# Performance work log

Hardware: AMD Instinct MI355X
Metric: run time of the kernel (lower is better)

Reference implementation:

```python
import jax, jax.numpy as jnp
import numpy as np

HID = 64
NUM_LAYERS = 4
IN_DIM = 1
OUT_DIM = 1
LN_EPS = 1e-5


def setup_inputs() -> dict:
    key = jax.random.key(0)
    ks = jax.random.split(key, 2 * NUM_LAYERS + 5)
    B, S = 1024, 512
    inp = {"x": jax.random.normal(ks[0], (B, S, IN_DIM), dtype=jnp.float32)}
    # per-layer gate weights, stored as [in+H, 4H] (x @ W + b, equivalent to torch Linear)
    for l in range(NUM_LAYERS):
        in_dim = IN_DIM if l == 0 else HID
        fan_in = in_dim + HID
        bound = 1.0 / np.sqrt(fan_in)
        inp[f"W{l}"] = jax.random.uniform(ks[1 + 2 * l], (fan_in, 4 * HID), jnp.float32, -bound, bound)
        inp[f"b{l}"] = jax.random.uniform(ks[2 + 2 * l], (4 * HID,), jnp.float32, -bound, bound)
    inp["ln_g"] = jnp.ones((HID,), jnp.float32)
    inp["ln_b"] = jnp.zeros((HID,), jnp.float32)
    bo = 1.0 / np.sqrt(HID)
    inp["Wout"] = jax.random.uniform(ks[-2], (HID, OUT_DIM), jnp.float32, -bo, bo)
    inp["bout"] = jax.random.uniform(ks[-1], (OUT_DIM,), jnp.float32, -bo, bo)
    return inp


def _lstm_forward(x, Ws, bs):
    B = x.shape[0]
    h0 = tuple(jnp.zeros((B, HID), x.dtype) for _ in range(NUM_LAYERS))
    c0 = tuple(jnp.zeros((B, HID), x.dtype) for _ in range(NUM_LAYERS))

    def step(carry, xt):
        h, c = carry
        inp = xt
        new_h, new_c = [], []
        for l in range(NUM_LAYERS):
            z = jnp.concatenate([inp, h[l]], axis=-1) @ Ws[l] + bs[l]  # [B, 4H]
            i, f, g, o = jnp.split(z, 4, axis=-1)
            i = jax.nn.sigmoid(i)
            f = jax.nn.sigmoid(f)
            g = jnp.tanh(g)
            o = jax.nn.sigmoid(o)
            c_new = f * c[l] + i * g
            h_new = o * jnp.tanh(c_new)
            new_h.append(h_new)
            new_c.append(c_new)
            inp = h_new
        return (tuple(new_h), tuple(new_c)), new_h[-1]

    xs = jnp.swapaxes(x, 0, 1)  # [S, B, in]
    _, outs = jax.lax.scan(step, (h0, c0), xs)
    return jnp.swapaxes(outs, 0, 1)  # [B, S, H]


def reference(x, W0, b0, W1, b1, W2, b2, W3, b3, ln_g, ln_b, Wout, bout):
    Ws = (W0, W1, W2, W3)
    bs = (b0, b1, b2, b3)
    out = _lstm_forward(x, Ws, bs)  # [B, S, H]
    mu = jnp.mean(out, axis=-1, keepdims=True)
    var = jnp.mean(jnp.square(out - mu), axis=-1, keepdims=True)
    normed = (out - mu) * jax.lax.rsqrt(var + LN_EPS) * ln_g + ln_b
    return normed @ Wout + bout  # [B, S, 1]
```

## Files before the change

kernel.cpp:

```cpp
#include <hip/hip_runtime.h>

#define SEQ   512
#define NTHR  1024
#define NBLK  256

typedef _Float16 f16x8 __attribute__((ext_vector_type(8)));
typedef float    f32x4 __attribute__((ext_vector_type(4)));

#define MFMA(a, b, c) __builtin_amdgcn_mfma_f32_16x16x32_f16((a), (b), (c), 0, 0, 0)

__device__ __forceinline__ float sig_(float x) {
    return __builtin_amdgcn_rcpf(1.0f + __builtin_amdgcn_exp2f(x * -1.4426950408889634f));
}
__device__ __forceinline__ float tanh_(float x) {
    return fmaf(2.0f, __builtin_amdgcn_rcpf(1.0f + __builtin_amdgcn_exp2f(x * -2.8853900817779268f)), -1.0f);
}

__global__ __launch_bounds__(NTHR, 4) void lstm4_pipe16b(
    const float* __restrict__ x,
    const float* __restrict__ W0, const float* __restrict__ B0,
    const float* __restrict__ W1, const float* __restrict__ B1,
    const float* __restrict__ W2, const float* __restrict__ B2,
    const float* __restrict__ W3, const float* __restrict__ B3,
    const float* __restrict__ ln_g, const float* __restrict__ ln_b,
    const float* __restrict__ Wout, const float* __restrict__ bout,
    float* __restrict__ out)
{
    __shared__ __align__(16) _Float16 hbuf[2][4][4][64];
    __shared__ float xall[4][SEQ];
    __shared__ float part[16][4][4][3];
    __shared__ float sconst[2];

    const int tid  = threadIdx.x;
    const int lane = tid & 63;
    const int w    = tid >> 6;
    const int ell  = w >> 2;
    const int om   = w & 3;
    const int lam  = lane >> 4;
    const int bc   = lane & 15;
    const int br   = bc & 3;
    const int k    = bc >> 2;
    const int bb   = blockIdx.x;

    for (int i = tid; i < 4 * SEQ; i += NTHR)
        xall[i >> 9][i & 511] = x[bb * 4 * SEQ + i];
    for (int i = tid; i < 2 * 4 * 4 * 64; i += NTHR)
        ((_Float16*)hbuf)[i] = (_Float16)0.0f;

    if (tid < 64) {
        float a = ln_g[tid] * Wout[tid];
        float b = ln_b[tid] * Wout[tid];
#pragma unroll
        for (int off = 32; off > 0; off >>= 1) {
            a += __shfl_xor(a, off, 64);
            b += __shfl_xor(b, off, 64);
        }
        if (tid == 0) { sconst[0] = a; sconst[1] = b; }
    }

    const float* Wp = (ell == 0) ? W0 : (ell == 1) ? W1 : (ell == 2) ? W2 : W3;
    const float* Bp = (ell == 0) ? B0 : (ell == 1) ? B1 : (ell == 2) ? B2 : B3;

    f16x8 wf[4][4];
    f32x4 biasv[4];
#pragma unroll
    for (int i = 0; i < 4; ++i) {
        const int T  = om * 4 + i;
        const int cA = (bc & 3) * 64 + T * 4 + (bc >> 2);
        if (ell == 0) {
#pragma unroll
            for (int kt = 0; kt < 2; ++kt)
#pragma unroll
                for (int e = 0; e < 8; ++e)
                    wf[i][kt][e] = (_Float16)W0[(1 + kt * 32 + lam * 8 + e) * 256 + cA];
#pragma unroll
            for (int e = 0; e < 8; ++e) { wf[i][2][e] = (_Float16)0.0f; wf[i][3][e] = (_Float16)0.0f; }
            if (lam == 0) wf[i][2][0] = (_Float16)W0[cA];
        } else {
#pragma unroll
            for (int kt = 0; kt < 4; ++kt)
#pragma unroll
                for (int e = 0; e < 8; ++e)
                    wf[i][kt][e] = (_Float16)Wp[(kt * 32 + lam * 8 + e) * 256 + cA];
        }
#pragma unroll
        for (int r = 0; r < 4; ++r)
            biasv[i][r] = Bp[r * 64 + T * 4 + lam];
    }

    const int   mK  = (om * 4 + k) * 4 + lam;
    const float gwK = ln_g[mK] * Wout[mK];
    const int   wrK = br * 128 + (((mK >> 3) ^ br) * 16) + (mK & 7) * 2;

    const int a0 = br * 128 + ((lam)     ^ br) * 16;
    const int a1 = br * 128 + ((4 + lam) ^ br) * 16;

    const bool k1b = (bc & 4) != 0;
    const bool k2b = (bc & 8) != 0;

    float cstK = 0.0f;
    char* const hb = (char*)hbuf;

    __syncthreads();
    const float Sgw = sconst[0];
    const float Sbw = sconst[1] + bout[0];

    for (int tau = 0; tau < SEQ + 3; ++tau) {
        const char* bR = hb + (((tau + 1) & 1) ? 2048 : 0);
        char*       bW = hb + (((tau    ) & 1) ? 2048 : 0);
        const int  t      = tau - ell;
        const bool active = (t >= 0) && (t < SEQ);

        if (active) {
            f16x8 b0, b1, b2, b3;
            if (ell == 0) {
                b0 = *(const f16x8*)(bR + a0);
                b1 = *(const f16x8*)(bR + a1);
                f16x8 xf;
#pragma unroll
                for (int e = 0; e < 8; ++e) xf[e] = (_Float16)0.0f;
                if (lam == 0) xf[0] = (_Float16)xall[br][t];
                b2 = xf; b3 = xf;
            } else {
                const char* bIn   = bR + (ell - 1) * 512;
                const char* bSelf = bR + ell * 512;
                b0 = *(const f16x8*)(bIn + a0);
                b1 = *(const f16x8*)(bIn + a1);
                b2 = *(const f16x8*)(bSelf + a0);
                b3 = *(const f16x8*)(bSelf + a1);
            }

            f32x4 A0 = MFMA(wf[0][0], b0, biasv[0]);
            f32x4 A1 = MFMA(wf[1][0], b0, biasv[1]);
            f32x4 A2 = MFMA(wf[2][0], b0, biasv[2]);
            f32x4 A3 = MFMA(wf[3][0], b0, biasv[3]);
            A0 = MFMA(wf[0][1], b1, A0);  A1 = MFMA(wf[1][1], b1, A1);
            A2 = MFMA(wf[2][1], b1, A2);  A3 = MFMA(wf[3][1], b1, A3);
            A0 = MFMA(wf[0][2], b2, A0);  A1 = MFMA(wf[1][2], b2, A1);
            A2 = MFMA(wf[2][2], b2, A2);  A3 = MFMA(wf[3][2], b2, A3);
            A0 = MFMA(wf[0][3], b3, A0);  A1 = MFMA(wf[1][3], b3, A1);
            A2 = MFMA(wf[2][3], b3, A2);  A3 = MFMA(wf[3][3], b3, A3);

            const f32x4 s01 = k1b ? A1 : A0;
            const f32x4 s23 = k1b ? A3 : A2;
            const f32x4 aK  = k2b ? s23 : s01;

            const float gi = sig_(aK[0]);
            const float gf = sig_(aK[1]);
            const float gg = tanh_(aK[2]);
            const float go = sig_(aK[3]);
            cstK = fmaf(gf, cstK, gi * gg);
            const float hn = go * tanh_(cstK);
            *(_Float16*)(bW + ell * 512 + wrK) = (_Float16)hn;

            if (ell == 3) {
                float v1 = hn, v2 = hn * hn, v3 = hn * gwK;
                v1 += __shfl_xor(v1, 4, 64);  v2 += __shfl_xor(v2, 4, 64);  v3 += __shfl_xor(v3, 4, 64);
                v1 += __shfl_xor(v1, 8, 64);  v2 += __shfl_xor(v2, 8, 64);  v3 += __shfl_xor(v3, 8, 64);
                v1 += __shfl_xor(v1, 16, 64); v2 += __shfl_xor(v2, 16, 64); v3 += __shfl_xor(v3, 16, 64);
                v1 += __shfl_xor(v1, 32, 64); v2 += __shfl_xor(v2, 32, 64); v3 += __shfl_xor(v3, 32, 64);
                if (bc < 4) {
                    float* pp = &part[t & 15][om][bc][0];
                    pp[0] = v1; pp[1] = v2; pp[2] = v3;
                }
            }
        }
        __syncthreads();

        const int t3 = tau - 3;
        if (t3 >= 7 && (t3 & 7) == 7) {
            const int row = tid >> 4, sub = tid & 15;
            if (row < 32) {
                const int sl = row >> 2, b = row & 3;
                const int slot = (t3 - 7 + sl) & 15;
                float u1 = part[slot][sub & 3][b][0];
                float u2 = part[slot][sub & 3][b][1];
                float u3 = part[slot][sub & 3][b][2];
                u1 += __shfl_xor(u1, 1, 64); u2 += __shfl_xor(u2, 1, 64); u3 += __shfl_xor(u3, 1, 64);
                u1 += __shfl_xor(u1, 2, 64); u2 += __shfl_xor(u2, 2, 64); u3 += __shfl_xor(u3, 2, 64);
                if (sub == 0) {
                    const float mu = u1 * (1.0f / 64.0f);
                    float var = fmaf(u2, 1.0f / 64.0f, -mu * mu);
                    var = fmaxf(var, 0.0f);
                    const float rs = rsqrtf(var + 1e-5f);
                    out[(bb * 4 + b) * SEQ + (t3 - 7) + sl] = fmaf(rs, fmaf(-mu, Sgw, u3), Sbw);
                }
            }
        }
    }
}

extern "C" void kernel_launch(void* const* d_in, const int* in_sizes, int n_in,
                              void* d_out, int out_size, void* d_ws, size_t ws_size,
                              hipStream_t stream)
{
    const float* x    = (const float*)d_in[0];
    const float* W0   = (const float*)d_in[1];
    const float* B0   = (const float*)d_in[2];
    const float* W1   = (const float*)d_in[3];
    const float* B1   = (const float*)d_in[4];
    const float* W2   = (const float*)d_in[5];
    const float* B2   = (const float*)d_in[6];
    const float* W3   = (const float*)d_in[7];
    const float* B3   = (const float*)d_in[8];
    const float* ln_g = (const float*)d_in[9];
    const float* ln_b = (const float*)d_in[10];
    const float* Wout = (const float*)d_in[11];
    const float* bout = (const float*)d_in[12];
    float* out = (float*)d_out;

    lstm4_pipe16b<<<NBLK, NTHR, 0, stream>>>(x, W0, B0, W1, B1, W2, B2, W3, B3,
                                             ln_g, ln_b, Wout, bout, out);
}
```

Measured before the change: 560.6 us.

## Give each wave a whole LSTM layer with a deeper skewed pipeline

The block shrinks from 16 waves to 4, so each wave owns one full layer and computes all 16 gate tiles sequentially. The layer stagger grows to two steps, and the hidden state moves to a 4-slot LDS ring, so a block barrier is needed only every other step. The layer-norm and output projection are now done inside the last-layer wave with shuffles, which removes the shared partial-sum buffer and the separate reduction phase. In exchange each wave holds 4x the weight registers, which risks spills or AGPR use, and there is less wave-level parallelism to hide MFMA and transcendental latency.

```diff
diff --git a/kernel.cpp b/kernel.cpp
--- a/kernel.cpp
+++ b/kernel.cpp
@@ -1,7 +1,7 @@
 #include <hip/hip_runtime.h>
 
 #define SEQ   512
-#define NTHR  1024
+#define NTHR  256
 #define NBLK  256
 
 typedef _Float16 f16x8 __attribute__((ext_vector_type(8)));
@@ -16,7 +16,7 @@
     return fmaf(2.0f, __builtin_amdgcn_rcpf(1.0f + __builtin_amdgcn_exp2f(x * -2.8853900817779268f)), -1.0f);
 }
 
-__global__ __launch_bounds__(NTHR, 4) void lstm4_pipe16b(
+__global__ __launch_bounds__(NTHR, 1) void lstm4_deep(
     const float* __restrict__ x,
     const float* __restrict__ W0, const float* __restrict__ B0,
     const float* __restrict__ W1, const float* __restrict__ B1,
@@ -26,25 +26,22 @@
     const float* __restrict__ Wout, const float* __restrict__ bout,
     float* __restrict__ out)
 {
-    __shared__ __align__(16) _Float16 hbuf[2][4][4][64];
+    __shared__ __align__(16) _Float16 hbuf[4][4][4][64];
     __shared__ float xall[4][SEQ];
-    __shared__ float part[16][4][4][3];
     __shared__ float sconst[2];
 
     const int tid  = threadIdx.x;
     const int lane = tid & 63;
-    const int w    = tid >> 6;
-    const int ell  = w >> 2;
-    const int om   = w & 3;
+    const int ell  = tid >> 6;
     const int lam  = lane >> 4;
     const int bc   = lane & 15;
     const int br   = bc & 3;
-    const int k    = bc >> 2;
+    const int kq   = bc >> 2;
     const int bb   = blockIdx.x;
 
     for (int i = tid; i < 4 * SEQ; i += NTHR)
         xall[i >> 9][i & 511] = x[bb * 4 * SEQ + i];
-    for (int i = tid; i < 2 * 4 * 4 * 64; i += NTHR)
+    for (int i = tid; i < 4 * 4 * 4 * 64; i += NTHR)
         ((_Float16*)hbuf)[i] = (_Float16)0.0f;
 
     if (tid < 64) {
@@ -61,132 +58,125 @@
     const float* Wp = (ell == 0) ? W0 : (ell == 1) ? W1 : (ell == 2) ? W2 : W3;
     const float* Bp = (ell == 0) ? B0 : (ell == 1) ? B1 : (ell == 2) ? B2 : B3;
 
-    f16x8 wf[4][4];
-    f32x4 biasv[4];
-#pragma unroll
-    for (int i = 0; i < 4; ++i) {
-        const int T  = om * 4 + i;
+    f16x8 wf[16][4];
+    f32x4 biasv[16];
+#pragma unroll
+    for (int T = 0; T < 16; ++T) {
         const int cA = (bc & 3) * 64 + T * 4 + (bc >> 2);
         if (ell == 0) {
 #pragma unroll
             for (int kt = 0; kt < 2; ++kt)
 #pragma unroll
                 for (int e = 0; e < 8; ++e)
-                    wf[i][kt][e] = (_Float16)W0[(1 + kt * 32 + lam * 8 + e) * 256 + cA];
-#pragma unroll
-            for (int e = 0; e < 8; ++e) { wf[i][2][e] = (_Float16)0.0f; wf[i][3][e] = (_Float16)0.0f; }
-            if (lam == 0) wf[i][2][0] = (_Float16)W0[cA];
+                    wf[T][kt][e] = (_Float16)W0[(1 + kt * 32 + lam * 8 + e) * 256 + cA];
+#pragma unroll
+            for (int e = 0; e < 8; ++e) { wf[T][2][e] = (_Float16)0.0f; wf[T][3][e] = (_Float16)0.0f; }
+            if (lam == 0) wf[T][2][0] = (_Float16)W0[cA];
         } else {
 #pragma unroll
             for (int kt = 0; kt < 4; ++kt)
 #pragma unroll
                 for (int e = 0; e < 8; ++e)
-                    wf[i][kt][e] = (_Float16)Wp[(kt * 32 + lam * 8 + e) * 256 + cA];
+                    wf[T][kt][e] = (_Float16)Wp[(kt * 32 + lam * 8 + e) * 256 + cA];
         }
 #pragma unroll
         for (int r = 0; r < 4; ++r)
-            biasv[i][r] = Bp[r * 64 + T * 4 + lam];
-    }
-
-    const int   mK  = (om * 4 + k) * 4 + lam;
-    const float gwK = ln_g[mK] * Wout[mK];
-    const int   wrK = br * 128 + (((mK >> 3) ^ br) * 16) + (mK & 7) * 2;
+            biasv[T][r] = Bp[r * 64 + T * 4 + lam];
+    }
+
+    float gwv[4];
+    int   wrg[4];
+#pragma unroll
+    for (int g = 0; g < 4; ++g) {
+        const int m = (g * 4 + kq) * 4 + lam;
+        gwv[g] = ln_g[m] * Wout[m];
+        wrg[g] = br * 128 + (((m >> 3) ^ br) * 16) + (m & 7) * 2;
+    }
 
     const int a0 = br * 128 + ((lam)     ^ br) * 16;
     const int a1 = br * 128 + ((4 + lam) ^ br) * 16;
-
     const bool k1b = (bc & 4) != 0;
     const bool k2b = (bc & 8) != 0;
 
-    float cstK = 0.0f;
+    float cst[4] = {0.f, 0.f, 0.f, 0.f};
     char* const hb = (char*)hbuf;
 
     __syncthreads();
     const float Sgw = sconst[0];
     const float Sbw = sconst[1] + bout[0];
 
-    for (int tau = 0; tau < SEQ + 3; ++tau) {
-        const char* bR = hb + (((tau + 1) & 1) ? 2048 : 0);
-        char*       bW = hb + (((tau    ) & 1) ? 2048 : 0);
-        const int  t      = tau - ell;
-        const bool active = (t >= 0) && (t < SEQ);
-
-        if (active) {
+    for (int tau = 0; tau < SEQ + 6; ++tau) {
+        const int t = tau - 2 * ell;
+        if (t >= 0 && t < SEQ) {
+            const char* selfB = hb + ((((tau - 1) & 3) * 4 + ell) * 512);
             f16x8 b0, b1, b2, b3;
             if (ell == 0) {
-                b0 = *(const f16x8*)(bR + a0);
-                b1 = *(const f16x8*)(bR + a1);
+                b0 = *(const f16x8*)(selfB + a0);
+                b1 = *(const f16x8*)(selfB + a1);
                 f16x8 xf;
 #pragma unroll
                 for (int e = 0; e < 8; ++e) xf[e] = (_Float16)0.0f;
                 if (lam == 0) xf[0] = (_Float16)xall[br][t];
                 b2 = xf; b3 = xf;
             } else {
-                const char* bIn   = bR + (ell - 1) * 512;
-                const char* bSelf = bR + ell * 512;
-                b0 = *(const f16x8*)(bIn + a0);
-                b1 = *(const f16x8*)(bIn + a1);
-                b2 = *(const f16x8*)(bSelf + a0);
-                b3 = *(const f16x8*)(bSelf + a1);
+                const char* inB = hb + ((((tau - 2) & 3) * 4 + (ell - 1)) * 512);
+                b0 = *(const f16x8*)(inB + a0);
+                b1 = *(const f16x8*)(inB + a1);
+                b2 = *(const f16x8*)(selfB + a0);
+                b3 = *(const f16x8*)(selfB + a1);
             }
 
-            f32x4 A0 = MFMA(wf[0][0], b0, biasv[0]);
-            f32x4 A1 = MFMA(wf[1][0], b0, biasv[1]);
-            f32x4 A2 = MFMA(wf[2][0], b0, biasv[2]);
-            f32x4 A3 = MFMA(wf[3][0], b0, biasv[3]);
-            A0 = MFMA(wf[0][1], b1, A0);  A1 = MFMA(wf[1][1], b1, A1);
-            A2 = MFMA(wf[2][1], b1, A2);  A3 = MFMA(wf[3][1], b1, A3);
-            A0 = MFMA(wf[0][2], b2, A0);  A1 = MFMA(wf[1][2], b2, A1);
-            A2 = MFMA(wf[2][2], b2, A2);  A3 = MFMA(wf[3][2], b2, A3);
-            A0 = MFMA(wf[0][3], b3, A0);  A1 = MFMA(wf[1][3], b3, A1);
-            A2 = MFMA(wf[2][3], b3, A2);  A3 = MFMA(wf[3][3], b3, A3);
-
-            const f32x4 s01 = k1b ? A1 : A0;
-            const f32x4 s23 = k1b ? A3 : A2;
-            const f32x4 aK  = k2b ? s23 : s01;
-
-            const float gi = sig_(aK[0]);
-            const float gf = sig_(aK[1]);
-            const float gg = tanh_(aK[2]);
-            const float go = sig_(aK[3]);
-            cstK = fmaf(gf, cstK, gi * gg);
-            const float hn = go * tanh_(cstK);
-            *(_Float16*)(bW + ell * 512 + wrK) = (_Float16)hn;
+            char* hw = hb + (((tau & 3) * 4 + ell) * 512);
+            float s1 = 0.0f, s2 = 0.0f, s3 = 0.0f;
+
+#pragma unroll
+            for (int g = 0; g < 4; ++g) {
+                f32x4 A0 = MFMA(wf[4 * g + 0][0], b0, biasv[4 * g + 0]);
+                f32x4 A1 = MFMA(wf[4 * g + 1][0], b0, biasv[4 * g + 1]);
+                f32x4 A2 = MFMA(wf[4 * g + 2][0], b0, biasv[4 * g + 2]);
+                f32x4 A3 = MFMA(wf[4 * g + 3][0], b0, biasv[4 * g + 3]);
+                A0 = MFMA(wf[4 * g + 0][1], b1, A0);
+                A1 = MFMA(wf[4 * g + 1][1], b1, A1);
+                A2 = MFMA(wf[4 * g + 2][1], b1, A2);
+                A3 = MFMA(wf[4 * g + 3][1], b1, A3);
+                A0 = MFMA(wf[4 * g + 0][2], b2, A0);
+                A1 = MFMA(wf[4 * g + 1][2], b2, A1);
+                A2 = MFMA(wf[4 * g + 2][2], b2, A2);
+                A3 = MFMA(wf[4 * g + 3][2], b2, A3);
+                if (ell != 0) {
+                    A0 = MFMA(wf[4 * g + 0][3], b3, A0);
+                    A1 = MFMA(wf[4 * g + 1][3], b3, A1);
+                    A2 = MFMA(wf[4 * g + 2][3], b3, A2);
+                    A3 = MFMA(wf[4 * g + 3][3], b3, A3);
+                }
+                const f32x4 s01 = k1b ? A1 : A0;
+                const f32x4 s23 = k1b ? A3 : A2;
+                const f32x4 aK  = k2b ? s23 : s01;
+                const float gi = sig_(aK[0]);
+                const float gf = sig_(aK[1]);
+                const float gg = tanh_(aK[2]);
+                const float go = sig_(aK[3]);
+                cst[g] = fmaf(gf, cst[g], gi * gg);
+                const float hn = go * tanh_(cst[g]);
+                *(_Float16*)(hw + wrg[g]) = (_Float16)hn;
+                if (ell == 3) { s1 += hn; s2 = fmaf(hn, hn, s2); s3 = fmaf(hn, gwv[g], s3); }
+            }
 
             if (ell == 3) {
-                float v1 = hn, v2 = hn * hn, v3 = hn * gwK;
-                v1 += __shfl_xor(v1, 4, 64);  v2 += __shfl_xor(v2, 4, 64);  v3 += __shfl_xor(v3, 4, 64);
-                v1 += __shfl_xor(v1, 8, 64);  v2 += __shfl_xor(v2, 8, 64);  v3 += __shfl_xor(v3, 8, 64);
-                v1 += __shfl_xor(v1, 16, 64); v2 += __shfl_xor(v2, 16, 64); v3 += __shfl_xor(v3, 16, 64);
-                v1 += __shfl_xor(v1, 32, 64); v2 += __shfl_xor(v2, 32, 64); v3 += __shfl_xor(v3, 32, 64);
-                if (bc < 4) {
-                    float* pp = &part[t & 15][om][bc][0];
-                    pp[0] = v1; pp[1] = v2; pp[2] = v3;
+                s1 += __shfl_xor(s1, 4, 64);  s2 += __shfl_xor(s2, 4, 64);  s3 += __shfl_xor(s3, 4, 64);
+                s1 += __shfl_xor(s1, 8, 64);  s2 += __shfl_xor(s2, 8, 64);  s3 += __shfl_xor(s3, 8, 64);
+                s1 += __shfl_xor(s1, 16, 64); s2 += __shfl_xor(s2, 16, 64); s3 += __shfl_xor(s3, 16, 64);
+                s1 += __shfl_xor(s1, 32, 64); s2 += __shfl_xor(s2, 32, 64); s3 += __shfl_xor(s3, 32, 64);
+                if (lane < 4) {
+                    const float mu = s1 * (1.0f / 64.0f);
+                    float var = fmaf(s2, 1.0f / 64.0f, -mu * mu);
+                    var = fmaxf(var, 0.0f);
+                    const float rs = rsqrtf(var + 1e-5f);
+                    out[(bb * 4 + lane) * SEQ + t] = fmaf(rs, fmaf(-mu, Sgw, s3), Sbw);
                 }
             }
         }
-        __syncthreads();
-
-        const int t3 = tau - 3;
-        if (t3 >= 7 && (t3 & 7) == 7) {
-            const int row = tid >> 4, sub = tid & 15;
-            if (row < 32) {
-                const int sl = row >> 2, b = row & 3;
-                const int slot = (t3 - 7 + sl) & 15;
-                float u1 = part[slot][sub & 3][b][0];
-                float u2 = part[slot][sub & 3][b][1];
-                float u3 = part[slot][sub & 3][b][2];
-                u1 += __shfl_xor(u1, 1, 64); u2 += __shfl_xor(u2, 1, 64); u3 += __shfl_xor(u3, 1, 64);
-                u1 += __shfl_xor(u1, 2, 64); u2 += __shfl_xor(u2, 2, 64); u3 += __shfl_xor(u3, 2, 64);
-                if (sub == 0) {
-                    const float mu = u1 * (1.0f / 64.0f);
-                    float var = fmaf(u2, 1.0f / 64.0f, -mu * mu);
-                    var = fmaxf(var, 0.0f);
-                    const float rs = rsqrtf(var + 1e-5f);
-                    out[(bb * 4 + b) * SEQ + (t3 - 7) + sl] = fmaf(rs, fmaf(-mu, Sgw, u3), Sbw);
-                }
-            }
-        }
+        if (tau & 1) __syncthreads();
     }
 }
 
@@ -209,6 +199,6 @@
     const float* bout = (const float*)d_in[12];
     float* out = (float*)d_out;
 
-    lstm4_pipe16b<<<NBLK, NTHR, 0, stream>>>(x, W0, B0, W1, B1, W2, B2, W3, B3,
-                                             ln_g, ln_b, Wout, bout, out);
-}
+    lstm4_deep<<<NBLK, NTHR, 0, stream>>>(x, W0, B0, W1, B1, W2, B2, W3, B3,
+                                          ln_g, ln_b, Wout, bout, out);
+}
```

After: 759.4 us. +35.4%, slower.

## Peel pipeline prologue/epilogue, unroll steady state by four, skip layer-0 zero MFMAs

Applied to the files above, without the earlier changes.

The time loop is split into a checked prologue, an unchecked steady-state loop unrolled by four with constant double-buffer offsets, and a checked epilogue. The layer-norm combine step is placed at a fixed position inside the unrolled body. Layer 0 skips the four MFMAs whose weight fragments are all zero except the x term, which now goes into the third k-tile. MFMA issue is wrapped in s_setprio. The goal is to remove per-step branch and address arithmetic and wasted matrix work on the serial recurrence, at the cost of larger code and more complex control flow.

```diff
diff --git a/kernel.cpp b/kernel.cpp
--- a/kernel.cpp
+++ b/kernel.cpp
@@ -16,7 +16,86 @@
     return fmaf(2.0f, __builtin_amdgcn_rcpf(1.0f + __builtin_amdgcn_exp2f(x * -2.8853900817779268f)), -1.0f);
 }
 
-__global__ __launch_bounds__(NTHR, 4) void lstm4_pipe16b(
+#define TICK(RD, WR, TAU, CHECKED)                                             \
+    {                                                                          \
+        const int t = (TAU) - ell;                                             \
+        if (!(CHECKED) || ((unsigned)t < (unsigned)SEQ)) {                     \
+            f16x8 b0, b1, b2, b3;                                              \
+            if (ell == 0) {                                                    \
+                b0 = *(const f16x8*)(hb + aSelf0 + (RD));                      \
+                b1 = *(const f16x8*)(hb + aSelf1 + (RD));                      \
+                f16x8 xf;                                                      \
+                _Pragma("unroll")                                              \
+                for (int e = 0; e < 8; ++e) xf[e] = (_Float16)0.0f;            \
+                if (lam == 0) xf[0] = (_Float16)xrow[t];                       \
+                b2 = xf; b3 = xf;                                              \
+            } else {                                                           \
+                b0 = *(const f16x8*)(hb + aIn0 + (RD));                        \
+                b1 = *(const f16x8*)(hb + aIn1 + (RD));                        \
+                b2 = *(const f16x8*)(hb + aSelf0 + (RD));                      \
+                b3 = *(const f16x8*)(hb + aSelf1 + (RD));                      \
+            }                                                                  \
+            __builtin_amdgcn_s_setprio(1);                                     \
+            f32x4 A0 = MFMA(wf[0][0], b0, biasv[0]);                           \
+            f32x4 A1 = MFMA(wf[1][0], b0, biasv[1]);                           \
+            f32x4 A2 = MFMA(wf[2][0], b0, biasv[2]);                           \
+            f32x4 A3 = MFMA(wf[3][0], b0, biasv[3]);                           \
+            A0 = MFMA(wf[0][1], b1, A0);  A1 = MFMA(wf[1][1], b1, A1);         \
+            A2 = MFMA(wf[2][1], b1, A2);  A3 = MFMA(wf[3][1], b1, A3);         \
+            A0 = MFMA(wf[0][2], b2, A0);  A1 = MFMA(wf[1][2], b2, A1);         \
+            A2 = MFMA(wf[2][2], b2, A2);  A3 = MFMA(wf[3][2], b2, A3);         \
+            if (ell != 0) {                                                    \
+                A0 = MFMA(wf[0][3], b3, A0);  A1 = MFMA(wf[1][3], b3, A1);     \
+                A2 = MFMA(wf[2][3], b3, A2);  A3 = MFMA(wf[3][3], b3, A3);     \
+            }                                                                  \
+            __builtin_amdgcn_s_setprio(0);                                     \
+            const f32x4 s01 = k1b ? A1 : A0;                                   \
+            const f32x4 s23 = k1b ? A3 : A2;                                   \
+            const f32x4 aK  = k2b ? s23 : s01;                                 \
+            const float gi = sig_(aK[0]);                                      \
+            const float gf = sig_(aK[1]);                                      \
+            const float gg = tanh_(aK[2]);                                     \
+            const float go = sig_(aK[3]);                                      \
+            cstK = fmaf(gf, cstK, gi * gg);                                    \
+            const float hn = go * tanh_(cstK);                                 \
+            *(_Float16*)(hb + wrKS + (WR)) = (_Float16)hn;                     \
+            if (ell == 3) {                                                    \
+                float v1 = hn, v2 = hn * hn, v3 = hn * gwK;                    \
+                v1 += __shfl_xor(v1, 4, 64);  v2 += __shfl_xor(v2, 4, 64);  v3 += __shfl_xor(v3, 4, 64);  \
+                v1 += __shfl_xor(v1, 8, 64);  v2 += __shfl_xor(v2, 8, 64);  v3 += __shfl_xor(v3, 8, 64);  \
+                v1 += __shfl_xor(v1, 16, 64); v2 += __shfl_xor(v2, 16, 64); v3 += __shfl_xor(v3, 16, 64); \
+                v1 += __shfl_xor(v1, 32, 64); v2 += __shfl_xor(v2, 32, 64); v3 += __shfl_xor(v3, 32, 64); \
+                if (bc < 4) {                                                  \
+                    float* pp = &part[t & 15][om][bc][0];                      \
+                    pp[0] = v1; pp[1] = v2; pp[2] = v3;                        \
+                }                                                              \
+            }                                                                  \
+        }                                                                      \
+        __syncthreads();                                                       \
+    }
+
+#define COMBINE(T3)                                                            \
+    {                                                                          \
+        const int row = tid >> 4, sub = tid & 15;                              \
+        if (row < 32) {                                                        \
+            const int sl = row >> 2, b = row & 3;                              \
+            const int slot = ((T3) - 7 + sl) & 15;                             \
+            float u1 = part[slot][sub & 3][b][0];                              \
+            float u2 = part[slot][sub & 3][b][1];                              \
+            float u3 = part[slot][sub & 3][b][2];                              \
+            u1 += __shfl_xor(u1, 1, 64); u2 += __shfl_xor(u2, 1, 64); u3 += __shfl_xor(u3, 1, 64); \
+            u1 += __shfl_xor(u1, 2, 64); u2 += __shfl_xor(u2, 2, 64); u3 += __shfl_xor(u3, 2, 64); \
+            if (sub == 0) {                                                    \
+                const float mu = u1 * (1.0f / 64.0f);                          \
+                float var = fmaf(u2, 1.0f / 64.0f, -mu * mu);                  \
+                var = fmaxf(var, 0.0f);                                        \
+                const float rs = rsqrtf(var + 1e-5f);                         \
+                out[(bb * 4 + b) * SEQ + ((T3) - 7) + sl] = fmaf(rs, fmaf(-mu, Sgw, u3), Sbw); \
+            }                                                                  \
+        }                                                                      \
+    }
+
+__global__ __launch_bounds__(NTHR, 4) void lstm4_pipe16c(
     const float* __restrict__ x,
     const float* __restrict__ W0, const float* __restrict__ B0,
     const float* __restrict__ W1, const float* __restrict__ B1,
@@ -39,7 +118,7 @@
     const int lam  = lane >> 4;
     const int bc   = lane & 15;
     const int br   = bc & 3;
-    const int k    = bc >> 2;
+    const int kq   = bc >> 2;
     const int bb   = blockIdx.x;
 
     for (int i = tid; i < 4 * SEQ; i += NTHR)
@@ -88,12 +167,19 @@
             biasv[i][r] = Bp[r * 64 + T * 4 + lam];
     }
 
-    const int   mK  = (om * 4 + k) * 4 + lam;
+    const int   mK  = (om * 4 + kq) * 4 + lam;
     const float gwK = ln_g[mK] * Wout[mK];
     const int   wrK = br * 128 + (((mK >> 3) ^ br) * 16) + (mK & 7) * 2;
 
     const int a0 = br * 128 + ((lam)     ^ br) * 16;
     const int a1 = br * 128 + ((4 + lam) ^ br) * 16;
+
+    const int offIn   = (ell == 0) ? 0 : (ell - 1) * 512;
+    const int offSelf = ell * 512;
+    const int aIn0 = a0 + offIn,   aIn1 = a1 + offIn;
+    const int aSelf0 = a0 + offSelf, aSelf1 = a1 + offSelf;
+    const int wrKS = wrK + offSelf;
+    const float* const xrow = &xall[br][0];
 
     const bool k1b = (bc & 4) != 0;
     const bool k2b = (bc & 8) != 0;
@@ -105,88 +191,29 @@
     const float Sgw = sconst[0];
     const float Sbw = sconst[1] + bout[0];
 
-    for (int tau = 0; tau < SEQ + 3; ++tau) {
-        const char* bR = hb + (((tau + 1) & 1) ? 2048 : 0);
-        char*       bW = hb + (((tau    ) & 1) ? 2048 : 0);
-        const int  t      = tau - ell;
-        const bool active = (t >= 0) && (t < SEQ);
-
-        if (active) {
-            f16x8 b0, b1, b2, b3;
-            if (ell == 0) {
-                b0 = *(const f16x8*)(bR + a0);
-                b1 = *(const f16x8*)(bR + a1);
-                f16x8 xf;
-#pragma unroll
-                for (int e = 0; e < 8; ++e) xf[e] = (_Float16)0.0f;
-                if (lam == 0) xf[0] = (_Float16)xall[br][t];
-                b2 = xf; b3 = xf;
-            } else {
-                const char* bIn   = bR + (ell - 1) * 512;
-                const char* bSelf = bR + ell * 512;
-                b0 = *(const f16x8*)(bIn + a0);
-                b1 = *(const f16x8*)(bIn + a1);
-                b2 = *(const f16x8*)(bSelf + a0);
-                b3 = *(const f16x8*)(bSelf + a1);
-            }
-
-            f32x4 A0 = MFMA(wf[0][0], b0, biasv[0]);
-            f32x4 A1 = MFMA(wf[1][0], b0, biasv[1]);
-            f32x4 A2 = MFMA(wf[2][0], b0, biasv[2]);
-            f32x4 A3 = MFMA(wf[3][0], b0, biasv[3]);
-            A0 = MFMA(wf[0][1], b1, A0);  A1 = MFMA(wf[1][1], b1, A1);
-            A2 = MFMA(wf[2][1], b1, A2);  A3 = MFMA(wf[3][1], b1, A3);
-            A0 = MFMA(wf[0][2], b2, A0);  A1 = MFMA(wf[1][2], b2, A1);
-            A2 = MFMA(wf[2][2], b2, A2);  A3 = MFMA(wf[3][2], b2, A3);
-            A0 = MFMA(wf[0][3], b3, A0);  A1 = MFMA(wf[1][3], b3, A1);
-            A2 = MFMA(wf[2][3], b3, A2);  A3 = MFMA(wf[3][3], b3, A3);
-
-            const f32x4 s01 = k1b ? A1 : A0;
-            const f32x4 s23 = k1b ? A3 : A2;
-            const f32x4 aK  = k2b ? s23 : s01;
-
-            const float gi = sig_(aK[0]);
-            const float gf = sig_(aK[1]);
-            const float gg = tanh_(aK[2]);
-            const float go = sig_(aK[3]);
-            cstK = fmaf(gf, cstK, gi * gg);
-            const float hn = go * tanh_(cstK);
-            *(_Float16*)(bW + ell * 512 + wrK) = (_Float16)hn;
-
-            if (ell == 3) {
-                float v1 = hn, v2 = hn * hn, v3 = hn * gwK;
-                v1 += __shfl_xor(v1, 4, 64);  v2 += __shfl_xor(v2, 4, 64);  v3 += __shfl_xor(v3, 4, 64);
-                v1 += __shfl_xor(v1, 8, 64);  v2 += __shfl_xor(v2, 8, 64);  v3 += __shfl_xor(v3, 8, 64);
-                v1 += __shfl_xor(v1, 16, 64); v2 += __shfl_xor(v2, 16, 64); v3 += __shfl_xor(v3, 16, 64);
-                v1 += __shfl_xor(v1, 32, 64); v2 += __shfl_xor(v2, 32, 64); v3 += __shfl_xor(v3, 32, 64);
-                if (bc < 4) {
-                    float* pp = &part[t & 15][om][bc][0];
-                    pp[0] = v1; pp[1] = v2; pp[2] = v3;
-                }
-            }
-        }
-        __syncthreads();
-
+    for (int tau = 0; tau < 4; ++tau) {
+        const int RDp = ((tau + 1) & 1) * 2048;
+        const int WRp = (tau & 1) * 2048;
+        TICK(RDp, WRp, tau, true)
         const int t3 = tau - 3;
-        if (t3 >= 7 && (t3 & 7) == 7) {
-            const int row = tid >> 4, sub = tid & 15;
-            if (row < 32) {
-                const int sl = row >> 2, b = row & 3;
-                const int slot = (t3 - 7 + sl) & 15;
-                float u1 = part[slot][sub & 3][b][0];
-                float u2 = part[slot][sub & 3][b][1];
-                float u3 = part[slot][sub & 3][b][2];
-                u1 += __shfl_xor(u1, 1, 64); u2 += __shfl_xor(u2, 1, 64); u3 += __shfl_xor(u3, 1, 64);
-                u1 += __shfl_xor(u1, 2, 64); u2 += __shfl_xor(u2, 2, 64); u3 += __shfl_xor(u3, 2, 64);
-                if (sub == 0) {
-                    const float mu = u1 * (1.0f / 64.0f);
-                    float var = fmaf(u2, 1.0f / 64.0f, -mu * mu);
-                    var = fmaxf(var, 0.0f);
-                    const float rs = rsqrtf(var + 1e-5f);
-                    out[(bb * 4 + b) * SEQ + (t3 - 7) + sl] = fmaf(rs, fmaf(-mu, Sgw, u3), Sbw);
-                }
-            }
-        }
+        if (t3 >= 7 && (t3 & 7) == 7) COMBINE(t3)
+    }
+
+    for (int j = 0; j < 127; ++j) {
+        const int tbase = 4 + 4 * j;
+        TICK(2048, 0, tbase + 0, false)
+        TICK(0, 2048, tbase + 1, false)
+        TICK(2048, 0, tbase + 2, false)
+        if ((tbase & 7) == 0) COMBINE(tbase - 1)
+        TICK(0, 2048, tbase + 3, false)
+    }
+
+    for (int tau = SEQ; tau < SEQ + 3; ++tau) {
+        const int RDp = ((tau + 1) & 1) * 2048;
+        const int WRp = (tau & 1) * 2048;
+        TICK(RDp, WRp, tau, true)
+        const int t3 = tau - 3;
+        if (t3 >= 7 && (t3 & 7) == 7) COMBINE(t3)
     }
 }
 
@@ -209,6 +236,6 @@
     const float* bout = (const float*)d_in[12];
     float* out = (float*)d_out;
 
-    lstm4_pipe16b<<<NBLK, NTHR, 0, stream>>>(x, W0, B0, W1, B1, W2, B2, W3, B3,
+    lstm4_pipe16c<<<NBLK, NTHR, 0, stream>>>(x, W0, B0, W1, B1, W2, B2, W3, B3,
                                              ln_g, ln_b, Wout, bout, out);
 }
```

Result: slower. 856.6 us (+52.8%).

## Replace per-step block barriers with per-layer atomic progress flags

Applied to the files above, without the earlier changes.

Replaces the global __syncthreads wavefront pipeline with dataflow synchronization. Each layer's four waves bump a shared-memory progress counter with release atomics, and consumers spin with acquire loads on their own layer, the upstream layer and the downstream layer. The h buffer grows to four time slots so layers can run up to a few steps apart. The aim is to remove full-block barrier stalls so layers proceed as soon as their inputs are ready, at the cost of spin-wait overhead and a risk of LDS ordering subtleties.

```diff
diff --git a/kernel.cpp b/kernel.cpp
--- a/kernel.cpp
+++ b/kernel.cpp
@@ -3,6 +3,7 @@
 #define SEQ   512
 #define NTHR  1024
 #define NBLK  256
+#define WGS __HIP_MEMORY_SCOPE_WORKGROUP
 
 typedef _Float16 f16x8 __attribute__((ext_vector_type(8)));
 typedef float    f32x4 __attribute__((ext_vector_type(4)));
@@ -16,7 +17,7 @@
     return fmaf(2.0f, __builtin_amdgcn_rcpf(1.0f + __builtin_amdgcn_exp2f(x * -2.8853900817779268f)), -1.0f);
 }
 
-__global__ __launch_bounds__(NTHR, 4) void lstm4_pipe16b(
+__global__ __launch_bounds__(NTHR, 4) void lstm4_flow(
     const float* __restrict__ x,
     const float* __restrict__ W0, const float* __restrict__ B0,
     const float* __restrict__ W1, const float* __restrict__ B1,
@@ -26,10 +27,11 @@
     const float* __restrict__ Wout, const float* __restrict__ bout,
     float* __restrict__ out)
 {
-    __shared__ __align__(16) _Float16 hbuf[2][4][4][64];
+    __shared__ __align__(16) _Float16 hbuf[4][4][4][64];
     __shared__ float xall[4][SEQ];
     __shared__ float part[16][4][4][3];
     __shared__ float sconst[2];
+    __shared__ int   prog[4][16];
 
     const int tid  = threadIdx.x;
     const int lane = tid & 63;
@@ -39,13 +41,14 @@
     const int lam  = lane >> 4;
     const int bc   = lane & 15;
     const int br   = bc & 3;
-    const int k    = bc >> 2;
+    const int kq   = bc >> 2;
     const int bb   = blockIdx.x;
 
     for (int i = tid; i < 4 * SEQ; i += NTHR)
         xall[i >> 9][i & 511] = x[bb * 4 * SEQ + i];
-    for (int i = tid; i < 2 * 4 * 4 * 64; i += NTHR)
+    for (int i = tid; i < 4 * 4 * 4 * 64; i += NTHR)
         ((_Float16*)hbuf)[i] = (_Float16)0.0f;
+    if (tid < 4) prog[tid][0] = 0;
 
     if (tid < 64) {
         float a = ln_g[tid] * Wout[tid];
@@ -88,7 +91,7 @@
             biasv[i][r] = Bp[r * 64 + T * 4 + lam];
     }
 
-    const int   mK  = (om * 4 + k) * 4 + lam;
+    const int   mK  = (om * 4 + kq) * 4 + lam;
     const float gwK = ln_g[mK] * Wout[mK];
     const int   wrK = br * 128 + (((mK >> 3) ^ br) * 16) + (mK & 7) * 2;
 
@@ -98,93 +101,106 @@
     const bool k1b = (bc & 4) != 0;
     const bool k2b = (bc & 8) != 0;
 
+    f16x8 xf;
+#pragma unroll
+    for (int e = 0; e < 8; ++e) xf[e] = (_Float16)0.0f;
+
     float cstK = 0.0f;
     char* const hb = (char*)hbuf;
+
+    int* const pOwn = &prog[ell][0];
+    int* const pIn  = &prog[(ell > 0) ? ell - 1 : 0][0];
+    int* const pDn  = &prog[(ell < 3) ? ell + 1 : 3][0];
 
     __syncthreads();
     const float Sgw = sconst[0];
     const float Sbw = sconst[1] + bout[0];
 
-    for (int tau = 0; tau < SEQ + 3; ++tau) {
-        const char* bR = hb + (((tau + 1) & 1) ? 2048 : 0);
-        char*       bW = hb + (((tau    ) & 1) ? 2048 : 0);
-        const int  t      = tau - ell;
-        const bool active = (t >= 0) && (t < SEQ);
-
-        if (active) {
-            f16x8 b0, b1, b2, b3;
-            if (ell == 0) {
-                b0 = *(const f16x8*)(bR + a0);
-                b1 = *(const f16x8*)(bR + a1);
-                f16x8 xf;
-#pragma unroll
-                for (int e = 0; e < 8; ++e) xf[e] = (_Float16)0.0f;
-                if (lam == 0) xf[0] = (_Float16)xall[br][t];
-                b2 = xf; b3 = xf;
-            } else {
-                const char* bIn   = bR + (ell - 1) * 512;
-                const char* bSelf = bR + ell * 512;
-                b0 = *(const f16x8*)(bIn + a0);
-                b1 = *(const f16x8*)(bIn + a1);
-                b2 = *(const f16x8*)(bSelf + a0);
-                b3 = *(const f16x8*)(bSelf + a1);
+    for (int t = 0; t < SEQ; ++t) {
+        const int t4 = 4 * t;
+
+        while (__hip_atomic_load(pOwn, __ATOMIC_ACQUIRE, WGS) < t4) {}
+        if (ell > 0)
+            while (__hip_atomic_load(pIn, __ATOMIC_ACQUIRE, WGS) < t4 + 4) {}
+        if (ell < 3 && t >= 4)
+            while (__hip_atomic_load(pDn, __ATOMIC_ACQUIRE, WGS) < t4 - 12) {}
+        __builtin_amdgcn_sched_barrier(0);
+
+        const int sW = ((t & 3) * 4 + ell) * 512;
+        const int sS = (((t - 1) & 3) * 4 + ell) * 512;
+
+        f16x8 b0, b1, b2, b3;
+        if (ell == 0) {
+            b0 = *(const f16x8*)(hb + sS + a0);
+            b1 = *(const f16x8*)(hb + sS + a1);
+            if (lam == 0) xf[0] = (_Float16)xall[br][t];
+            b2 = xf; b3 = xf;
+        } else {
+            const int sI = ((t & 3) * 4 + (ell - 1)) * 512;
+            b0 = *(const f16x8*)(hb + sI + a0);
+            b1 = *(const f16x8*)(hb + sI + a1);
+            b2 = *(const f16x8*)(hb + sS + a0);
+            b3 = *(const f16x8*)(hb + sS + a1);
+        }
+
+        f32x4 A0 = MFMA(wf[0][0], b0, biasv[0]);
+        f32x4 A1 = MFMA(wf[1][0], b0, biasv[1]);
+        f32x4 A2 = MFMA(wf[2][0], b0, biasv[2]);
+        f32x4 A3 = MFMA(wf[3][0], b0, biasv[3]);
+        A0 = MFMA(wf[0][1], b1, A0);  A1 = MFMA(wf[1][1], b1, A1);
+        A2 = MFMA(wf[2][1], b1, A2);  A3 = MFMA(wf[3][1], b1, A3);
+        A0 = MFMA(wf[0][2], b2, A0);  A1 = MFMA(wf[1][2], b2, A1);
+        A2 = MFMA(wf[2][2], b2, A2);  A3 = MFMA(wf[3][2], b2, A3);
+        A0 = MFMA(wf[0][3], b3, A0);  A1 = MFMA(wf[1][3], b3, A1);
+        A2 = MFMA(wf[2][3], b3, A2);  A3 = MFMA(wf[3][3], b3, A3);
+
+        const f32x4 s01 = k1b ? A1 : A0;
+        const f32x4 s23 = k1b ? A3 : A2;
+        const f32x4 aK  = k2b ? s23 : s01;
+
+        const float gi = sig_(aK[0]);
+        const float gf = sig_(aK[1]);
+        const float gg = tanh_(aK[2]);
+        const float go = sig_(aK[3]);
+        cstK = fmaf(gf, cstK, gi * gg);
+        const float hn = go * tanh_(cstK);
+        *(_Float16*)(hb + sW + wrK) = (_Float16)hn;
+
+        if (ell == 3) {
+            float v1 = hn, v2 = hn * hn, v3 = hn * gwK;
+            v1 += __shfl_xor(v1, 4, 64);  v2 += __shfl_xor(v2, 4, 64);  v3 += __shfl_xor(v3, 4, 64);
+            v1 += __shfl_xor(v1, 8, 64);  v2 += __shfl_xor(v2, 8, 64);  v3 += __shfl_xor(v3, 8, 64);
+            v1 += __shfl_xor(v1, 16, 64); v2 += __shfl_xor(v2, 16, 64); v3 += __shfl_xor(v3, 16, 64);
+            v1 += __shfl_xor(v1, 32, 64); v2 += __shfl_xor(v2, 32, 64); v3 += __shfl_xor(v3, 32, 64);
+            if (bc < 4) {
+                float* pp = &part[t & 15][om][bc][0];
+                pp[0] = v1; pp[1] = v2; pp[2] = v3;
             }
-
-            f32x4 A0 = MFMA(wf[0][0], b0, biasv[0]);
-            f32x4 A1 = MFMA(wf[1][0], b0, biasv[1]);
-            f32x4 A2 = MFMA(wf[2][0], b0, biasv[2]);
-            f32x4 A3 = MFMA(wf[3][0], b0, biasv[3]);
-            A0 = MFMA(wf[0][1], b1, A0);  A1 = MFMA(wf[1][1], b1, A1);
-            A2 = MFMA(wf[2][1], b1, A2);  A3 = MFMA(wf[3][1], b1, A3);
-            A0 = MFMA(wf[0][2], b2, A0);  A1 = MFMA(wf[1][2], b2, A1);
-            A2 = MFMA(wf[2][2], b2, A2);  A3 = MFMA(wf[3][2], b2, A3);
-            A0 = MFMA(wf[0][3], b3, A0);  A1 = MFMA(wf[1][3], b3, A1);
-            A2 = MFMA(wf[2][3], b3, A2);  A3 = MFMA(wf[3][3], b3, A3);
-
-            const f32x4 s01 = k1b ? A1 : A0;
-            const f32x4 s23 = k1b ? A3 : A2;
-            const f32x4 aK  = k2b ? s23 : s01;
-
-            const float gi = sig_(aK[0]);
-            const float gf = sig_(aK[1]);
-            const float gg = tanh_(aK[2]);
-            const float go = sig_(aK[3]);
-            cstK = fmaf(gf, cstK, gi * gg);
-            const float hn = go * tanh_(cstK);
-            *(_Float16*)(bW + ell * 512 + wrK) = (_Float16)hn;
-
-            if (ell == 3) {
-                float v1 = hn, v2 = hn * hn, v3 = hn * gwK;
-                v1 += __shfl_xor(v1, 4, 64);  v2 += __shfl_xor(v2, 4, 64);  v3 += __shfl_xor(v3, 4, 64);
-                v1 += __shfl_xor(v1, 8, 64);  v2 += __shfl_xor(v2, 8, 64);  v3 += __shfl_xor(v3, 8, 64);
-                v1 += __shfl_xor(v1, 16, 64); v2 += __shfl_xor(v2, 16, 64); v3 += __shfl_xor(v3, 16, 64);
-                v1 += __shfl_xor(v1, 32, 64); v2 += __shfl_xor(v2, 32, 64); v3 += __shfl_xor(v3, 32, 64);
-                if (bc < 4) {
-                    float* pp = &part[t & 15][om][bc][0];
-                    pp[0] = v1; pp[1] = v2; pp[2] = v3;
-                }
-            }
-        }
-        __syncthreads();
-
-        const int t3 = tau - 3;
-        if (t3 >= 7 && (t3 & 7) == 7) {
-            const int row = tid >> 4, sub = tid & 15;
-            if (row < 32) {
-                const int sl = row >> 2, b = row & 3;
-                const int slot = (t3 - 7 + sl) & 15;
-                float u1 = part[slot][sub & 3][b][0];
-                float u2 = part[slot][sub & 3][b][1];
-                float u3 = part[slot][sub & 3][b][2];
-                u1 += __shfl_xor(u1, 1, 64); u2 += __shfl_xor(u2, 1, 64); u3 += __shfl_xor(u3, 1, 64);
-                u1 += __shfl_xor(u1, 2, 64); u2 += __shfl_xor(u2, 2, 64); u3 += __shfl_xor(u3, 2, 64);
-                if (sub == 0) {
-                    const float mu = u1 * (1.0f / 64.0f);
-                    float var = fmaf(u2, 1.0f / 64.0f, -mu * mu);
-                    var = fmaxf(var, 0.0f);
-                    const float rs = rsqrtf(var + 1e-5f);
-                    out[(bb * 4 + b) * SEQ + (t3 - 7) + sl] = fmaf(rs, fmaf(-mu, Sgw, u3), Sbw);
-                }
+        }
+
+        if (lane == 0)
+            __hip_atomic_fetch_add(pOwn, 1, __ATOMIC_RELEASE, WGS);
+
+        if (ell == 3 && (t & 7) == 7) {
+            while (__hip_atomic_load(pOwn, __ATOMIC_ACQUIRE, WGS) < t4 + 4) {}
+            __builtin_amdgcn_sched_barrier(0);
+            const int s  = lane >> 5;
+            const int j  = lane & 31;
+            const int b  = (j >> 3) & 3;
+            const int o  = j & 3;
+            const int ts = t - 7 + 2 * om + s;
+            const int sl = ts & 15;
+            float u1 = part[sl][o][b][0];
+            float u2 = part[sl][o][b][1];
+            float u3 = part[sl][o][b][2];
+            u1 += __shfl_xor(u1, 1, 64); u2 += __shfl_xor(u2, 1, 64); u3 += __shfl_xor(u3, 1, 64);
+            u1 += __shfl_xor(u1, 2, 64); u2 += __shfl_xor(u2, 2, 64); u3 += __shfl_xor(u3, 2, 64);
+            if ((j & 7) == 0) {
+                const float mu = u1 * (1.0f / 64.0f);
+                float var = fmaf(u2, 1.0f / 64.0f, -mu * mu);
+                var = fmaxf(var, 0.0f);
+                const float rs = rsqrtf(var + 1e-5f);
+                out[(bb * 4 + b) * SEQ + ts] = fmaf(rs, fmaf(-mu, Sgw, u3), Sbw);
             }
         }
     }
@@ -209,6 +225,6 @@
     const float* bout = (const float*)d_in[12];
     float* out = (float*)d_out;
 
-    lstm4_pipe16b<<<NBLK, NTHR, 0, stream>>>(x, W0, B0, W1, B1, W2, B2, W3, B3,
-                                             ln_g, ln_b, Wout, bout, out);
-}
+    lstm4_flow<<<NBLK, NTHR, 0, stream>>>(x, W0, B0, W1, B1, W2, B2, W3, B3,
+                                          ln_g, ln_b, Wout, bout, out);
+}
```

New measurement: 649.7 us. 1.16x slower.
